# Performance work log

Measured on AMD Instinct MI355X. Metric: run time of the kernel, lower is better.

The kernel has to match this reference:

```python
import jax, jax.numpy as jnp
import numpy as np

N = 100000       # nodes
E = 1600000      # edges
NFEAT = 256
NHID = 128
NCLASS = 40


def setup_inputs() -> dict:
    key = jax.random.key(0)
    ks = jax.random.split(key, 7)
    x = jax.random.normal(ks[0], (N, NFEAT), dtype=jnp.float32)
    edge_index = jax.random.randint(ks[1], (2, E), 0, N, dtype=jnp.int32)
    edge_weight = jax.random.uniform(ks[2], (E,), dtype=jnp.float32)
    # Glorot-style init as in PyG GCNConv.reset_parameters
    W1 = jax.random.normal(ks[3], (NFEAT, NHID), dtype=jnp.float32) * np.float32(1.0 / np.sqrt(NFEAT))
    b1 = jnp.zeros((NHID,), dtype=jnp.float32)
    W2 = jax.random.normal(ks[4], (NHID, NCLASS), dtype=jnp.float32) * np.float32(1.0 / np.sqrt(NHID))
    b2 = jnp.zeros((NCLASS,), dtype=jnp.float32)
    return {"x": x, "edge_index": edge_index, "edge_weight": edge_weight,
            "W1": W1, "b1": b1, "W2": W2, "b2": b2}


def gcn_conv(x, W, b, src, dst, ew, n):
    """PyG GCNConv with add_self_loops=True (self-loop weight 1), sym norm.

    Self-loop contribution is added analytically (norm_ii = deg_i^-1) so we
    never materialize the augmented edge list.
    """
    xw = x @ W                                            # [n, out]
    deg = jax.ops.segment_sum(ew, dst, num_segments=n) + 1.0  # +1 self loop
    dinv = jnp.where(deg > 0, jax.lax.rsqrt(deg), 0.0)    # deg^-1/2
    norm = dinv[src] * ew * dinv[dst]                     # [E]
    agg = jax.ops.segment_sum(norm[:, None] * xw[src], dst, num_segments=n)
    agg = agg + (dinv * dinv)[:, None] * xw               # self-loop term
    return agg + b


def reference(x, edge_index, edge_weight, W1, b1, W2, b2):
    n = x.shape[0]
    src, dst = edge_index[0], edge_index[1]
    h = jax.nn.relu(gcn_conv(x, W1, b1, src, dst, edge_weight, n))
    # dropout is identity in eval mode
    h = gcn_conv(h, W2, b2, src, dst, edge_weight, n)
    nrm = jnp.linalg.norm(h, axis=-1, keepdims=True)      # F.normalize p=2
    return h / jnp.maximum(nrm, 1e-12)
```

## Files before the change

### kernel.cpp

```cpp
#include <hip/hip_runtime.h>


typedef unsigned short u16;
typedef unsigned long long u64;
typedef __attribute__((ext_vector_type(8))) short short8;
typedef __attribute__((ext_vector_type(4))) float f32x4;

#define FIXSCALE 4194304.0f
#define HW2S 48
#define NSLAB 640
#define MAXBUCK 832

static __device__ inline u16 f2bf(float f) {
    unsigned u = __float_as_uint(f);
    return (u16)((u + 0x7fffu + ((u >> 16) & 1u)) >> 16);
}
static __device__ inline float bf2f(u16 h) { return __uint_as_float(((unsigned)h) << 16); }

__launch_bounds__(256)
__global__ void k_fat1(const float* __restrict__ x, const u16* __restrict__ wt_hi,
                       const u16* __restrict__ wt_lo, u16* __restrict__ xw1, int N,
                       const int* __restrict__ dst, int* __restrict__ cnt1,
                       int E, int gB, int EPB, int NBUCK) {
    __shared__ __align__(16) u16 Ah[128 * 40];
    __shared__ __align__(16) u16 Bh[128 * 40];
    __shared__ __align__(16) u16 Bl[128 * 40];

    if (blockIdx.x >= gB) {
        int b = blockIdx.x - gB;
        int* cnt = (int*)Ah;
        for (int j = threadIdx.x; j < NBUCK; j += 256) cnt[j] = 0;
        __syncthreads();
        int beg = b * EPB, end = min(beg + EPB, E);
        for (int i = beg + threadIdx.x; i < end; i += 256)
            atomicAdd(&cnt[dst[i] >> 7], 1);
        __syncthreads();
        for (int j = threadIdx.x; j < NBUCK; j += 256)
            cnt1[(size_t)b * NBUCK + j] = cnt[j];
        return;
    }

    const int t = threadIdx.x;
    const int w = t >> 6;
    const int lane = t & 63;
    const int lrow = lane & 15;
    const int lk = (lane >> 4) * 8;
    const int row0 = blockIdx.x * 128;

    f32x4 acc[2][8] = {};

    for (int kt = 0; kt < 8; ++kt) {
#pragma unroll
        for (int i = 0; i < 4; ++i) {
            int flat = t + i * 256;
            int r = flat >> 3, c4 = flat & 7;
            int gr = row0 + r;
            float4 v = make_float4(0.f, 0.f, 0.f, 0.f);
            if (gr < N) v = *(const float4*)(x + (size_t)gr * 256 + kt * 32 + c4 * 4);
            ushort4 vh;
            vh.x = f2bf(v.x);
            vh.y = f2bf(v.y);
            vh.z = f2bf(v.z);
            vh.w = f2bf(v.w);
            *(ushort4*)(Ah + r * 40 + c4 * 4) = vh;
        }
#pragma unroll
        for (int i = 0; i < 2; ++i) {
            int flat = t + i * 256;
            int n = flat >> 2, c = flat & 3;
            *(short8*)(Bh + n * 40 + c * 8) =
                *(const short8*)(wt_hi + (size_t)n * 256 + kt * 32 + c * 8);
            *(short8*)(Bl + n * 40 + c * 8) =
                *(const short8*)(wt_lo + (size_t)n * 256 + kt * 32 + c * 8);
        }
        __syncthreads();

        short8 a0 = *(const short8*)(Ah + (w * 32 + lrow) * 40 + lk);
        short8 a1 = *(const short8*)(Ah + (w * 32 + 16 + lrow) * 40 + lk);
#pragma unroll
        for (int ni = 0; ni < 8; ++ni) {
            short8 bh = *(const short8*)(Bh + (ni * 16 + lrow) * 40 + lk);
            short8 bl = *(const short8*)(Bl + (ni * 16 + lrow) * 40 + lk);
            acc[0][ni] = __builtin_amdgcn_mfma_f32_16x16x32_bf16(a0, bh, acc[0][ni], 0, 0, 0);
            acc[1][ni] = __builtin_amdgcn_mfma_f32_16x16x32_bf16(a1, bh, acc[1][ni], 0, 0, 0);
            acc[0][ni] = __builtin_amdgcn_mfma_f32_16x16x32_bf16(a0, bl, acc[0][ni], 0, 0, 0);
            acc[1][ni] = __builtin_amdgcn_mfma_f32_16x16x32_bf16(a1, bl, acc[1][ni], 0, 0, 0);
        }
        __syncthreads();
    }

#pragma unroll
    for (int mi = 0; mi < 2; ++mi) {
        int rbase = row0 + w * 32 + mi * 16 + (lane >> 4) * 4;
#pragma unroll
        for (int r = 0; r < 4; ++r) {
            int gr = rbase + r;
            if (gr < N) {
                u16* p = xw1 + (size_t)gr * 128 + (lane & 15);
#pragma unroll
                for (int ni = 0; ni < 8; ++ni) p[ni * 16] = f2bf(acc[mi][ni][r]);
            }
        }
    }
}

__launch_bounds__(NSLAB)
__global__ void k_s2a(int* __restrict__ cnt1, int* __restrict__ colTot, int NBUCK) {
    __shared__ int s[NSLAB];
    int j = blockIdx.x;
    int t = threadIdx.x;
    int v = cnt1[(size_t)t * NBUCK + j];
    s[t] = v;
    __syncthreads();
    for (int off = 1; off < NSLAB; off <<= 1) {
        int u = (t >= off) ? s[t - off] : 0;
        __syncthreads();
        s[t] += u;
        __syncthreads();
    }
    cnt1[(size_t)t * NBUCK + j] = s[t] - v;
    if (t == NSLAB - 1) colTot[j] = s[t];
}

__launch_bounds__(1024)
__global__ void k_s2b(const int* __restrict__ colTot, int* __restrict__ bucketBase,
                      int* __restrict__ rowp, int NBUCK, int N, int E) {
    __shared__ int s[1024];
    int t = threadIdx.x;
    int v = (t < NBUCK) ? colTot[t] : 0;
    s[t] = v;
    __syncthreads();
    for (int off = 1; off < 1024; off <<= 1) {
        int u = (t >= off) ? s[t - off] : 0;
        __syncthreads();
        s[t] += u;
        __syncthreads();
    }
    if (t < NBUCK) bucketBase[t] = s[t] - v;
    if (t == NBUCK - 1) bucketBase[NBUCK] = s[t];
    if (t == 0) rowp[N] = E;
}

__launch_bounds__(256)
__global__ void k_s3(const int* __restrict__ src, const int* __restrict__ dst,
                     const float* __restrict__ ew, const int* __restrict__ cnt1,
                     const int* __restrict__ bucketBase, u64* __restrict__ tmp,
                     int E, int EPB, int NBUCK) {
    __shared__ int ldsOff[MAXBUCK];
    int b = blockIdx.x, t = threadIdx.x;
    for (int j = t; j < NBUCK; j += 256)
        ldsOff[j] = bucketBase[j] + cnt1[(size_t)b * NBUCK + j];
    __syncthreads();
    int beg = b * EPB, end = min(beg + EPB, E);
    for (int i = beg + t; i < end; i += 256) {
        int d = dst[i];
        int slot = atomicAdd(&ldsOff[d >> 7], 1);
        unsigned fix = (unsigned)__float2uint_rn(ew[i] * FIXSCALE);
        tmp[slot] = ((u64)(unsigned)src[i] << 30) | ((u64)(d & 127) << 23) | fix;
    }
}

__launch_bounds__(256)
__global__ void k_s4(const u64* __restrict__ tmp, const int* __restrict__ bucketBase,
                     int* __restrict__ rowp, float* __restrict__ dinv,
                     int2* __restrict__ entries, int N) {
    __shared__ int cnt[128];
    __shared__ unsigned degfix[128];
    __shared__ int sc[128];
    __shared__ int nextOff[128];
    __shared__ float dl[128];
    int k = blockIdx.x, t = threadIdx.x;
    int base = bucketBase[k], endb = bucketBase[k + 1];
    if (t < 128) { cnt[t] = 0; degfix[t] = 0; }
    __syncthreads();
    for (int i = base + t; i < endb; i += 256) {
        u64 r = tmp[i];
        int lid = (int)(r >> 23) & 127;
        atomicAdd(&cnt[lid], 1);
        atomicAdd(&degfix[lid], (unsigned)(r & 0x7fffff));
    }
    __syncthreads();
    if (t < 128) sc[t] = cnt[t];
    __syncthreads();
    for (int off = 1; off < 128; off <<= 1) {
        int u = 0;
        if (t < 128 && t >= off) u = sc[t - off];
        __syncthreads();
        if (t < 128) sc[t] += u;
        __syncthreads();
    }
    if (t < 128) {
        int off0 = base + sc[t] - cnt[t];
        nextOff[t] = off0;
        float di = rsqrtf((float)degfix[t] * (1.0f / FIXSCALE) + 1.0f);
        dl[t] = di;
        int gn = k * 128 + t;
        if (gn < N) { rowp[gn] = off0; dinv[gn] = di; }
    }
    __syncthreads();
    for (int i = base + t; i < endb; i += 256) {
        u64 r = tmp[i];
        int lid = (int)(r >> 23) & 127;
        int slot = atomicAdd(&nextOff[lid], 1);
        float ew = (float)(unsigned)(r & 0x7fffff) * (1.0f / FIXSCALE);
        float w = ew * dl[lid];
        entries[slot] = make_int2((int)(r >> 30), __float_as_int(w));
    }
}

__global__ void k_wsplit(const float* __restrict__ W1, u16* __restrict__ wt_hi,
                         u16* __restrict__ wt_lo) {
    int idx = blockIdx.x * 256 + threadIdx.x;
    if (idx < 256 * 128) {
        int n = idx & 127, k = idx >> 7;
        float f = W1[idx];
        u16 h = f2bf(f);
        wt_hi[n * 256 + k] = h;
        wt_lo[n * 256 + k] = f2bf(f - bf2f(h));
    }
}

__launch_bounds__(256)
__global__ void k_gather1(const u16* __restrict__ xw1, const int2* __restrict__ entries,
                          const int* __restrict__ row, const float* __restrict__ dinv,
                          float* __restrict__ agg1, int N) {
    int g = (blockIdx.x * 256 + threadIdx.x) >> 5;
    if (g >= N) return;
    int j = (threadIdx.x & 31) * 4;
    float di = dinv[g];
    float d2 = di * di;
    ushort4 sv = *(const ushort4*)(xw1 + (size_t)g * 128 + j);
    float4 acc = make_float4(d2 * bf2f(sv.x), d2 * bf2f(sv.y),
                             d2 * bf2f(sv.z), d2 * bf2f(sv.w));
    int e = row[g], end = row[g + 1];
    for (; e + 2 <= end; e += 2) {
        int2 e0 = entries[e];
        int2 e1 = entries[e + 1];
        ushort4 v0 = *(const ushort4*)(xw1 + (size_t)e0.x * 128 + j);
        ushort4 v1 = *(const ushort4*)(xw1 + (size_t)e1.x * 128 + j);
        float w0 = __int_as_float(e0.y) * dinv[e0.x];
        float w1 = __int_as_float(e1.y) * dinv[e1.x];
        acc.x += w0 * bf2f(v0.x) + w1 * bf2f(v1.x);
        acc.y += w0 * bf2f(v0.y) + w1 * bf2f(v1.y);
        acc.z += w0 * bf2f(v0.z) + w1 * bf2f(v1.z);
        acc.w += w0 * bf2f(v0.w) + w1 * bf2f(v1.w);
    }
    if (e < end) {
        int2 e0 = entries[e];
        ushort4 v0 = *(const ushort4*)(xw1 + (size_t)e0.x * 128 + j);
        float w0 = __int_as_float(e0.y) * dinv[e0.x];
        acc.x += w0 * bf2f(v0.x);
        acc.y += w0 * bf2f(v0.y);
        acc.z += w0 * bf2f(v0.z);
        acc.w += w0 * bf2f(v0.w);
    }
    *(float4*)(agg1 + (size_t)g * 128 + j) = acc;
}

__launch_bounds__(320)
__global__ void k_gemm2(const float* __restrict__ agg1, const float* __restrict__ W2,
                        const float* __restrict__ b1, u16* __restrict__ hw2, int N) {
    __shared__ float As[64 * 132];
    __shared__ float Bs[128 * 40];
    const int t = threadIdx.x;
    const int row0 = blockIdx.x * 64;

    for (int flat = t; flat < 128 * 40; flat += 320) Bs[flat] = W2[flat];

#pragma unroll
    for (int i = 0; i < 7; ++i) {
        int flat = t + i * 320;
        if (flat < 2048) {
            int r = flat >> 5, c4 = flat & 31;
            int gr = row0 + r;
            float4 v = make_float4(0.f, 0.f, 0.f, 0.f);
            if (gr < N) {
                v = *(const float4*)(agg1 + (size_t)gr * 128 + c4 * 4);
                float4 bb = *(const float4*)(b1 + c4 * 4);
                v.x = fmaxf(v.x + bb.x, 0.f);
                v.y = fmaxf(v.y + bb.y, 0.f);
                v.z = fmaxf(v.z + bb.z, 0.f);
                v.w = fmaxf(v.w + bb.w, 0.f);
            }
            *(float4*)(As + r * 132 + c4 * 4) = v;
        }
    }
    __syncthreads();

    const int tx = t % 40;
    const int ty = t / 40;
    float acc[8];
#pragma unroll
    for (int r = 0; r < 8; ++r) acc[r] = 0.f;
    for (int k = 0; k < 128; ++k) {
        float b = Bs[k * 40 + tx];
#pragma unroll
        for (int r = 0; r < 8; ++r) acc[r] += As[(ty * 8 + r) * 132 + k] * b;
    }
#pragma unroll
    for (int r = 0; r < 8; ++r) {
        int gr = row0 + ty * 8 + r;
        if (gr < N) hw2[(size_t)gr * HW2S + tx] = f2bf(acc[r]);
    }
    for (int idx = t; idx < 64 * 8; idx += 320) {
        int r = idx >> 3, c = 40 + (idx & 7);
        int gr = row0 + r;
        if (gr < N) hw2[(size_t)gr * HW2S + c] = 0;
    }
}

__launch_bounds__(256)
__global__ void k_gather2(const u16* __restrict__ hw2, const int2* __restrict__ entries,
                          const int* __restrict__ row, const float* __restrict__ dinv,
                          const float* __restrict__ b2, float* __restrict__ out, int N) {
    int g = (blockIdx.x * 256 + threadIdx.x) >> 3;
    if (g >= N) return;
    int l = threadIdx.x & 7;
    int c0 = l * 6;
    float di = dinv[g];
    float d2 = di * di;
    float bb[6];
#pragma unroll
    for (int k = 0; k < 6; ++k) bb[k] = (c0 + k < 40) ? b2[c0 + k] : 0.f;

    float acc[6];
    {
        const u16* hn = hw2 + (size_t)g * HW2S + c0;
        ushort2 s0 = *(const ushort2*)(hn);
        ushort2 s1 = *(const ushort2*)(hn + 2);
        ushort2 s2 = *(const ushort2*)(hn + 4);
        acc[0] = d2 * bf2f(s0.x) + bb[0];
        acc[1] = d2 * bf2f(s0.y) + bb[1];
        acc[2] = d2 * bf2f(s1.x) + bb[2];
        acc[3] = d2 * bf2f(s1.y) + bb[3];
        acc[4] = d2 * bf2f(s2.x) + bb[4];
        acc[5] = d2 * bf2f(s2.y) + bb[5];
    }
    int e = row[g], end = row[g + 1];
    for (; e < end; ++e) {
        int2 ent = entries[e];
        float w = __int_as_float(ent.y) * dinv[ent.x];
        const u16* hr = hw2 + (size_t)ent.x * HW2S + c0;
        ushort2 v0 = *(const ushort2*)(hr);
        ushort2 v1 = *(const ushort2*)(hr + 2);
        ushort2 v2 = *(const ushort2*)(hr + 4);
        acc[0] += w * bf2f(v0.x);
        acc[1] += w * bf2f(v0.y);
        acc[2] += w * bf2f(v1.x);
        acc[3] += w * bf2f(v1.y);
        acc[4] += w * bf2f(v2.x);
        acc[5] += w * bf2f(v2.y);
    }
    float ss = 0.f;
#pragma unroll
    for (int k = 0; k < 6; ++k) ss += acc[k] * acc[k];
    ss += __shfl_xor(ss, 1);
    ss += __shfl_xor(ss, 2);
    ss += __shfl_xor(ss, 4);
    float inv = 1.f / fmaxf(sqrtf(ss), 1e-12f);
#pragma unroll
    for (int k = 0; k < 6; ++k) {
        int c = c0 + k;
        if (c < 40) out[(size_t)g * 40 + c] = acc[k] * inv;
    }
}

extern "C" void kernel_launch(void* const* d_in, const int* in_sizes, int n_in,
                              void* d_out, int out_size, void* d_ws, size_t ws_size,
                              hipStream_t stream) {
    const float* x   = (const float*)d_in[0];
    const int*   ei  = (const int*)d_in[1];
    const float* ew  = (const float*)d_in[2];
    const float* W1  = (const float*)d_in[3];
    const float* b1  = (const float*)d_in[4];
    const float* W2  = (const float*)d_in[5];
    const float* b2  = (const float*)d_in[6];
    float* out = (float*)d_out;

    const int N = in_sizes[0] / 256;
    const int E = in_sizes[2];
    const int* src = ei;
    const int* dst = ei + E;
    const int NBUCK = (N + 127) >> 7;
    const int EPB = (E + NSLAB - 1) / NSLAB;

    char* ws = (char*)d_ws;
    size_t off = 0;
    auto take = [&](size_t bytes) -> void* {
        void* p = (void*)(ws + off);
        off += (bytes + 255) & ~(size_t)255;
        return p;
    };
    int*   cnt1    = (int*)take((size_t)NSLAB * NBUCK * 4);
    int*   colTot  = (int*)take((size_t)NBUCK * 4);
    int*   bucketBase = (int*)take((size_t)(NBUCK + 1) * 4);
    int*   rowp    = (int*)take((size_t)(N + 1) * 4);
    float* dinv    = (float*)take((size_t)N * 4);
    u64*   tmp     = (u64*)take((size_t)E * 8);
    int2*  entries = (int2*)take((size_t)E * 8);
    u16*   wt_hi   = (u16*)take((size_t)128 * 256 * 2);
    u16*   wt_lo   = (u16*)take((size_t)128 * 256 * 2);
    u16*   xw1     = (u16*)take((size_t)N * 128 * 2);
    float* agg1    = (float*)take((size_t)N * 128 * 4);
    u16*   hw2     = (u16*)take((size_t)N * HW2S * 2);

    k_wsplit<<<(256 * 128 + 255) / 256, 256, 0, stream>>>(W1, wt_hi, wt_lo);

    const int gB = (N + 127) / 128;
    k_fat1<<<gB + NSLAB, 256, 0, stream>>>(x, wt_hi, wt_lo, xw1, N,
                                           dst, cnt1, E, gB, EPB, NBUCK);

    k_s2a<<<NBUCK, NSLAB, 0, stream>>>(cnt1, colTot, NBUCK);
    k_s2b<<<1, 1024, 0, stream>>>(colTot, bucketBase, rowp, NBUCK, N, E);
    k_s3<<<NSLAB, 256, 0, stream>>>(src, dst, ew, cnt1, bucketBase, tmp, E, EPB, NBUCK);
    k_s4<<<NBUCK, 256, 0, stream>>>(tmp, bucketBase, rowp, dinv, entries, N);

    k_gather1<<<(N * 32 + 255) / 256, 256, 0, stream>>>(xw1, entries, rowp, dinv, agg1, N);
    k_gemm2<<<(N + 63) / 64, 320, 0, stream>>>(agg1, W2, b1, hw2, N);
    k_gather2<<<(N * 8 + 255) / 256, 256, 0, stream>>>(hw2, entries, rowp, dinv, b2, out, N);
}
```

Before: 275.6 us.

## Fuse edge scatter into GEMM1 kernel, pad hw2 rows and prescale by dinv

Measured after the change: 246.6 us. -10.5%, faster.

```diff
diff --git a/kernel.cpp b/kernel.cpp
--- a/kernel.cpp
+++ b/kernel.cpp
@@ -7,7 +7,7 @@
 typedef __attribute__((ext_vector_type(4))) float f32x4;
 
 #define FIXSCALE 4194304.0f
-#define HW2S 48
+#define HW2S 64
 #define NSLAB 640
 #define MAXBUCK 832
 
@@ -18,25 +18,81 @@
 static __device__ inline float bf2f(u16 h) { return __uint_as_float(((unsigned)h) << 16); }
 
 __launch_bounds__(256)
-__global__ void k_fat1(const float* __restrict__ x, const u16* __restrict__ wt_hi,
-                       const u16* __restrict__ wt_lo, u16* __restrict__ xw1, int N,
-                       const int* __restrict__ dst, int* __restrict__ cnt1,
-                       int E, int gB, int EPB, int NBUCK) {
+__global__ void k_count(const int* __restrict__ dst, int* __restrict__ cnt1,
+                        int E, int EPB, int NBUCK) {
+    __shared__ int cnt[MAXBUCK];
+    int b = blockIdx.x;
+    for (int j = threadIdx.x; j < NBUCK; j += 256) cnt[j] = 0;
+    __syncthreads();
+    int beg = b * EPB, end = min(beg + EPB, E);
+    for (int i = beg + threadIdx.x; i < end; i += 256)
+        atomicAdd(&cnt[dst[i] >> 7], 1);
+    __syncthreads();
+    for (int j = threadIdx.x; j < NBUCK; j += 256)
+        cnt1[(size_t)b * NBUCK + j] = cnt[j];
+}
+
+__launch_bounds__(NSLAB)
+__global__ void k_s2a(int* __restrict__ cnt1, int* __restrict__ colTot, int NBUCK) {
+    __shared__ int s[NSLAB];
+    int j = blockIdx.x;
+    int t = threadIdx.x;
+    int v = cnt1[(size_t)t * NBUCK + j];
+    s[t] = v;
+    __syncthreads();
+    for (int off = 1; off < NSLAB; off <<= 1) {
+        int u = (t >= off) ? s[t - off] : 0;
+        __syncthreads();
+        s[t] += u;
+        __syncthreads();
+    }
+    cnt1[(size_t)t * NBUCK + j] = s[t] - v;
+    if (t == NSLAB - 1) colTot[j] = s[t];
+}
+
+__launch_bounds__(1024)
+__global__ void k_s2b(const int* __restrict__ colTot, int* __restrict__ bucketBase,
+                      int* __restrict__ rowp, int NBUCK, int N, int E) {
+    __shared__ int s[1024];
+    int t = threadIdx.x;
+    int v = (t < NBUCK) ? colTot[t] : 0;
+    s[t] = v;
+    __syncthreads();
+    for (int off = 1; off < 1024; off <<= 1) {
+        int u = (t >= off) ? s[t - off] : 0;
+        __syncthreads();
+        s[t] += u;
+        __syncthreads();
+    }
+    if (t < NBUCK) bucketBase[t] = s[t] - v;
+    if (t == NBUCK - 1) bucketBase[NBUCK] = s[t];
+    if (t == 0) rowp[N] = E;
+}
+
+__launch_bounds__(256)
+__global__ void k_fat(const float* __restrict__ x, const u16* __restrict__ wt_hi,
+                      const u16* __restrict__ wt_lo, u16* __restrict__ xw1, int N,
+                      const int* __restrict__ src, const int* __restrict__ dst,
+                      const float* __restrict__ ew, const int* __restrict__ cnt1,
+                      const int* __restrict__ bucketBase, u64* __restrict__ tmp,
+                      int E, int gB, int EPB, int NBUCK) {
     __shared__ __align__(16) u16 Ah[128 * 40];
     __shared__ __align__(16) u16 Bh[128 * 40];
     __shared__ __align__(16) u16 Bl[128 * 40];
 
     if (blockIdx.x >= gB) {
-        int b = blockIdx.x - gB;
-        int* cnt = (int*)Ah;
-        for (int j = threadIdx.x; j < NBUCK; j += 256) cnt[j] = 0;
+        int* ldsOff = (int*)Ah;
+        int b = blockIdx.x - gB, t = threadIdx.x;
+        for (int j = t; j < NBUCK; j += 256)
+            ldsOff[j] = bucketBase[j] + cnt1[(size_t)b * NBUCK + j];
         __syncthreads();
         int beg = b * EPB, end = min(beg + EPB, E);
-        for (int i = beg + threadIdx.x; i < end; i += 256)
-            atomicAdd(&cnt[dst[i] >> 7], 1);
-        __syncthreads();
-        for (int j = threadIdx.x; j < NBUCK; j += 256)
-            cnt1[(size_t)b * NBUCK + j] = cnt[j];
+        for (int i = beg + t; i < end; i += 256) {
+            int d = dst[i];
+            int slot = atomicAdd(&ldsOff[d >> 7], 1);
+            unsigned fix = (unsigned)__float2uint_rn(ew[i] * FIXSCALE);
+            tmp[slot] = ((u64)(unsigned)src[i] << 30) | ((u64)(d & 127) << 23) | fix;
+        }
         return;
     }
 
@@ -101,62 +157,6 @@
                 for (int ni = 0; ni < 8; ++ni) p[ni * 16] = f2bf(acc[mi][ni][r]);
             }
         }
-    }
-}
-
-__launch_bounds__(NSLAB)
-__global__ void k_s2a(int* __restrict__ cnt1, int* __restrict__ colTot, int NBUCK) {
-    __shared__ int s[NSLAB];
-    int j = blockIdx.x;
-    int t = threadIdx.x;
-    int v = cnt1[(size_t)t * NBUCK + j];
-    s[t] = v;
-    __syncthreads();
-    for (int off = 1; off < NSLAB; off <<= 1) {
-        int u = (t >= off) ? s[t - off] : 0;
-        __syncthreads();
-        s[t] += u;
-        __syncthreads();
-    }
-    cnt1[(size_t)t * NBUCK + j] = s[t] - v;
-    if (t == NSLAB - 1) colTot[j] = s[t];
-}
-
-__launch_bounds__(1024)
-__global__ void k_s2b(const int* __restrict__ colTot, int* __restrict__ bucketBase,
-                      int* __restrict__ rowp, int NBUCK, int N, int E) {
-    __shared__ int s[1024];
-    int t = threadIdx.x;
-    int v = (t < NBUCK) ? colTot[t] : 0;
-    s[t] = v;
-    __syncthreads();
-    for (int off = 1; off < 1024; off <<= 1) {
-        int u = (t >= off) ? s[t - off] : 0;
-        __syncthreads();
-        s[t] += u;
-        __syncthreads();
-    }
-    if (t < NBUCK) bucketBase[t] = s[t] - v;
-    if (t == NBUCK - 1) bucketBase[NBUCK] = s[t];
-    if (t == 0) rowp[N] = E;
-}
-
-__launch_bounds__(256)
-__global__ void k_s3(const int* __restrict__ src, const int* __restrict__ dst,
-                     const float* __restrict__ ew, const int* __restrict__ cnt1,
-                     const int* __restrict__ bucketBase, u64* __restrict__ tmp,
-                     int E, int EPB, int NBUCK) {
-    __shared__ int ldsOff[MAXBUCK];
-    int b = blockIdx.x, t = threadIdx.x;
-    for (int j = t; j < NBUCK; j += 256)
-        ldsOff[j] = bucketBase[j] + cnt1[(size_t)b * NBUCK + j];
-    __syncthreads();
-    int beg = b * EPB, end = min(beg + EPB, E);
-    for (int i = beg + t; i < end; i += 256) {
-        int d = dst[i];
-        int slot = atomicAdd(&ldsOff[d >> 7], 1);
-        unsigned fix = (unsigned)__float2uint_rn(ew[i] * FIXSCALE);
-        tmp[slot] = ((u64)(unsigned)src[i] << 30) | ((u64)(d & 127) << 23) | fix;
     }
 }
 
@@ -233,19 +233,25 @@
     float4 acc = make_float4(d2 * bf2f(sv.x), d2 * bf2f(sv.y),
                              d2 * bf2f(sv.z), d2 * bf2f(sv.w));
     int e = row[g], end = row[g + 1];
-    for (; e + 2 <= end; e += 2) {
+    for (; e + 4 <= end; e += 4) {
         int2 e0 = entries[e];
         int2 e1 = entries[e + 1];
+        int2 e2 = entries[e + 2];
+        int2 e3 = entries[e + 3];
         ushort4 v0 = *(const ushort4*)(xw1 + (size_t)e0.x * 128 + j);
         ushort4 v1 = *(const ushort4*)(xw1 + (size_t)e1.x * 128 + j);
+        ushort4 v2 = *(const ushort4*)(xw1 + (size_t)e2.x * 128 + j);
+        ushort4 v3 = *(const ushort4*)(xw1 + (size_t)e3.x * 128 + j);
         float w0 = __int_as_float(e0.y) * dinv[e0.x];
         float w1 = __int_as_float(e1.y) * dinv[e1.x];
-        acc.x += w0 * bf2f(v0.x) + w1 * bf2f(v1.x);
-        acc.y += w0 * bf2f(v0.y) + w1 * bf2f(v1.y);
-        acc.z += w0 * bf2f(v0.z) + w1 * bf2f(v1.z);
-        acc.w += w0 * bf2f(v0.w) + w1 * bf2f(v1.w);
-    }
-    if (e < end) {
+        float w2 = __int_as_float(e2.y) * dinv[e2.x];
+        float w3 = __int_as_float(e3.y) * dinv[e3.x];
+        acc.x += w0 * bf2f(v0.x) + w1 * bf2f(v1.x) + w2 * bf2f(v2.x) + w3 * bf2f(v3.x);
+        acc.y += w0 * bf2f(v0.y) + w1 * bf2f(v1.y) + w2 * bf2f(v2.y) + w3 * bf2f(v3.y);
+        acc.z += w0 * bf2f(v0.z) + w1 * bf2f(v1.z) + w2 * bf2f(v2.z) + w3 * bf2f(v3.z);
+        acc.w += w0 * bf2f(v0.w) + w1 * bf2f(v1.w) + w2 * bf2f(v2.w) + w3 * bf2f(v3.w);
+    }
+    for (; e < end; ++e) {
         int2 e0 = entries[e];
         ushort4 v0 = *(const ushort4*)(xw1 + (size_t)e0.x * 128 + j);
         float w0 = __int_as_float(e0.y) * dinv[e0.x];
@@ -259,7 +265,8 @@
 
 __launch_bounds__(320)
 __global__ void k_gemm2(const float* __restrict__ agg1, const float* __restrict__ W2,
-                        const float* __restrict__ b1, u16* __restrict__ hw2, int N) {
+                        const float* __restrict__ b1, const float* __restrict__ dinv,
+                        u16* __restrict__ hw2, int N) {
     __shared__ float As[64 * 132];
     __shared__ float Bs[128 * 40];
     const int t = threadIdx.x;
@@ -300,10 +307,10 @@
 #pragma unroll
     for (int r = 0; r < 8; ++r) {
         int gr = row0 + ty * 8 + r;
-        if (gr < N) hw2[(size_t)gr * HW2S + tx] = f2bf(acc[r]);
-    }
-    for (int idx = t; idx < 64 * 8; idx += 320) {
-        int r = idx >> 3, c = 40 + (idx & 7);
+        if (gr < N) hw2[(size_t)gr * HW2S + tx] = f2bf(dinv[gr] * acc[r]);
+    }
+    for (int idx = t; idx < 64 * 24; idx += 320) {
+        int r = idx / 24, c = 40 + idx % 24;
         int gr = row0 + r;
         if (gr < N) hw2[(size_t)gr * HW2S + c] = 0;
     }
@@ -316,52 +323,48 @@
     int g = (blockIdx.x * 256 + threadIdx.x) >> 3;
     if (g >= N) return;
     int l = threadIdx.x & 7;
-    int c0 = l * 6;
+    int c0 = l * 8;
     float di = dinv[g];
-    float d2 = di * di;
-    float bb[6];
-#pragma unroll
-    for (int k = 0; k < 6; ++k) bb[k] = (c0 + k < 40) ? b2[c0 + k] : 0.f;
-
-    float acc[6];
+    float bb[8];
+#pragma unroll
+    for (int k = 0; k < 8; ++k) bb[k] = (c0 + k < 40) ? b2[c0 + k] : 0.f;
+
+    float acc[8];
     {
-        const u16* hn = hw2 + (size_t)g * HW2S + c0;
-        ushort2 s0 = *(const ushort2*)(hn);
-        ushort2 s1 = *(const ushort2*)(hn + 2);
-        ushort2 s2 = *(const ushort2*)(hn + 4);
-        acc[0] = d2 * bf2f(s0.x) + bb[0];
-        acc[1] = d2 * bf2f(s0.y) + bb[1];
-        acc[2] = d2 * bf2f(s1.x) + bb[2];
-        acc[3] = d2 * bf2f(s1.y) + bb[3];
-        acc[4] = d2 * bf2f(s2.x) + bb[4];
-        acc[5] = d2 * bf2f(s2.y) + bb[5];
+        short8 sv = *(const short8*)(hw2 + (size_t)g * HW2S + c0);
+#pragma unroll
+        for (int k = 0; k < 8; ++k) acc[k] = di * bf2f((u16)sv[k]) + bb[k];
     }
     int e = row[g], end = row[g + 1];
-    for (; e < end; ++e) {
-        int2 ent = entries[e];
-        float w = __int_as_float(ent.y) * dinv[ent.x];
-        const u16* hr = hw2 + (size_t)ent.x * HW2S + c0;
-        ushort2 v0 = *(const ushort2*)(hr);
-        ushort2 v1 = *(const ushort2*)(hr + 2);
-        ushort2 v2 = *(const ushort2*)(hr + 4);
-        acc[0] += w * bf2f(v0.x);
-        acc[1] += w * bf2f(v0.y);
-        acc[2] += w * bf2f(v1.x);
-        acc[3] += w * bf2f(v1.y);
-        acc[4] += w * bf2f(v2.x);
-        acc[5] += w * bf2f(v2.y);
+    for (; e + 2 <= end; e += 2) {
+        int2 e0 = entries[e];
+        int2 e1 = entries[e + 1];
+        float w0 = __int_as_float(e0.y);
+        float w1 = __int_as_float(e1.y);
+        short8 v0 = *(const short8*)(hw2 + (size_t)e0.x * HW2S + c0);
+        short8 v1 = *(const short8*)(hw2 + (size_t)e1.x * HW2S + c0);
+#pragma unroll
+        for (int k = 0; k < 8; ++k)
+            acc[k] += w0 * bf2f((u16)v0[k]) + w1 * bf2f((u16)v1[k]);
+    }
+    if (e < end) {
+        int2 e0 = entries[e];
+        float w0 = __int_as_float(e0.y);
+        short8 v0 = *(const short8*)(hw2 + (size_t)e0.x * HW2S + c0);
+#pragma unroll
+        for (int k = 0; k < 8; ++k) acc[k] += w0 * bf2f((u16)v0[k]);
     }
     float ss = 0.f;
 #pragma unroll
-    for (int k = 0; k < 6; ++k) ss += acc[k] * acc[k];
+    for (int k = 0; k < 8; ++k) ss += acc[k] * acc[k];
     ss += __shfl_xor(ss, 1);
     ss += __shfl_xor(ss, 2);
     ss += __shfl_xor(ss, 4);
     float inv = 1.f / fmaxf(sqrtf(ss), 1e-12f);
-#pragma unroll
-    for (int k = 0; k < 6; ++k) {
-        int c = c0 + k;
-        if (c < 40) out[(size_t)g * 40 + c] = acc[k] * inv;
+    if (l < 5) {
+        float* q = out + (size_t)g * 40 + c0;
+        *(float4*)(q)     = make_float4(acc[0] * inv, acc[1] * inv, acc[2] * inv, acc[3] * inv);
+        *(float4*)(q + 4) = make_float4(acc[4] * inv, acc[5] * inv, acc[6] * inv, acc[7] * inv);
     }
 }
 
@@ -405,17 +408,18 @@
     u16*   hw2     = (u16*)take((size_t)N * HW2S * 2);
 
     k_wsplit<<<(256 * 128 + 255) / 256, 256, 0, stream>>>(W1, wt_hi, wt_lo);
-
-    const int gB = (N + 127) / 128;
-    k_fat1<<<gB + NSLAB, 256, 0, stream>>>(x, wt_hi, wt_lo, xw1, N,
-                                           dst, cnt1, E, gB, EPB, NBUCK);
-
+    k_count<<<NSLAB, 256, 0, stream>>>(dst, cnt1, E, EPB, NBUCK);
     k_s2a<<<NBUCK, NSLAB, 0, stream>>>(cnt1, colTot, NBUCK);
     k_s2b<<<1, 1024, 0, stream>>>(colTot, bucketBase, rowp, NBUCK, N, E);
-    k_s3<<<NSLAB, 256, 0, stream>>>(src, dst, ew, cnt1, bucketBase, tmp, E, EPB, NBUCK);
+
+    const int gB = (N + 127) / 128;
+    k_fat<<<gB + NSLAB, 256, 0, stream>>>(x, wt_hi, wt_lo, xw1, N,
+                                          src, dst, ew, cnt1, bucketBase, tmp,
+                                          E, gB, EPB, NBUCK);
+
     k_s4<<<NBUCK, 256, 0, stream>>>(tmp, bucketBase, rowp, dinv, entries, N);
 
     k_gather1<<<(N * 32 + 255) / 256, 256, 0, stream>>>(xw1, entries, rowp, dinv, agg1, N);
-    k_gemm2<<<(N + 63) / 64, 320, 0, stream>>>(agg1, W2, b1, hw2, N);
+    k_gemm2<<<(N + 63) / 64, 320, 0, stream>>>(agg1, W2, b1, dinv, hw2, N);
     k_gather2<<<(N * 8 + 255) / 256, 256, 0, stream>>>(hw2, entries, rowp, dinv, b2, out, N);
 }
```
